# Optimization experiments

Hardware: AMD Instinct MI355X
Metric: run time of the kernel (lower is better)

Reference implementation:

```python
import jax, jax.numpy as jnp
import numpy as np

CHANNEL_DIM = 256
RATE = 4
KSIZE = 2 * RATE - 1  # odd=True


def bilinear_kernel(size, normalize=False):
    factor = (size + 1) // 2
    center = factor - 1 if size % 2 == 1 else factor - 0.5
    og = np.ogrid[:size, :size]
    kern = (1 - abs(og[0] - center) / factor) * (1 - abs(og[1] - center) / factor)
    if normalize:
        kern = kern / kern.sum()
    return kern.astype(np.float32)


def setup_inputs() -> dict:
    key = jax.random.key(0)
    x = jax.random.normal(key, (4, CHANNEL_DIM, 64, 64), dtype=jnp.float32)
    # The torch module builds a [C, C, k, k] weight that is block-diagonal:
    # weight[c, c] = bilinear kernel, all cross-channel blocks are zero.
    # We store only the nonzero diagonal as a depthwise kernel [C, 1, k, k]
    # (OIHW with feature_group_count=C), which computes identical math.
    kern = jnp.asarray(bilinear_kernel(KSIZE, normalize=False))  # [k, k]
    weight = jnp.broadcast_to(kern[None, None], (CHANNEL_DIM, 1, KSIZE, KSIZE))
    return {"x": x, "weight": weight}


def reference(x, weight):
    # F.conv_transpose2d(x, W, stride=r) with no padding/output_padding is
    # equivalent to a cross-correlation of the input dilated by r (lhs_dilation)
    # with the spatially-flipped kernel and padding k-1 on each side.
    # The bilinear kernel is symmetric, so the flip is a no-op.
    k = weight.shape[-1]
    return jax.lax.conv_general_dilated(
        x, weight,
        window_strides=(1, 1),
        padding=((k - 1, k - 1), (k - 1, k - 1)),
        lhs_dilation=(RATE, RATE),
        dimension_numbers=("NCHW", "OIHW", "NCHW"),
        feature_group_count=CHANNEL_DIM,
    )  # -> [N, C, (H-1)*rate + k, (W-1)*rate + k] = [4, 256, 259, 259]
```

## Files before the change

### kernel.cpp

```cpp
#include <hip/hip_runtime.h>


#define IH 64
#define IW 64
#define OH 259
#define OW 259
#define OROW 67081

typedef float float4u __attribute__((ext_vector_type(4), aligned(4)));

__global__ __launch_bounds__(256) void upsample4x_strip(
    const float* __restrict__ x, float* __restrict__ out)
{
    const int lane  = threadIdx.x & 63;
    const int g     = blockIdx.x * 4 + (threadIdx.x >> 6);
    const int strip = g & 7;
    const int nc    = g >> 3;

    const int q0 = strip * 8;
    const int q1 = (strip == 7) ? 65 : q0 + 8;

    const float* __restrict__ xp = x + (size_t)nc * (IH * IW);
    float* __restrict__ ob = out + (size_t)nc * OROW;

    float xl = (q0 == 0) ? 0.0f : xp[(q0 - 1) * IW + lane];
    float xh = xp[q0 * IW + lane];
    float xlm = __shfl_up(xl, 1); if (lane == 0) xlm = 0.0f;
    float xhm = __shfl_up(xh, 1); if (lane == 0) xhm = 0.0f;

    for (int q = q0; q < q1; ++q) {
        const int qn = q + 1;
        float xn = 0.0f;
        if (qn < q1 && qn < IH) xn = xp[qn * IW + lane];

#pragma unroll
        for (int py = 0; py < 4; ++py) {
            const int oy = 4 * q + py;
            if (oy < OH) {
                const float wyl = 0.25f * (float)(3 - py);
                const float wyh = 0.25f * (float)(py + 1);
                float B = wyl * xl  + wyh * xh;
                float A = wyl * xlm + wyh * xhm;

                float e1 = 0.5f * (A + B);
                float e0 = 0.5f * (A + e1);
                float e2 = 0.5f * (e1 + B);

                float* rp = ob + (size_t)oy * OW;
                float4u v = {e0, e1, e2, B};
                ((float4u*)rp)[lane] = v;

                if (lane == 63) {
                    float4u t = {B, 0.75f * B, 0.5f * B, 0.25f * B};
                    *(float4u*)(rp + 255) = t;
                }
            }
        }

        xl = xh; xlm = xhm;
        xh = xn;
        xhm = __shfl_up(xh, 1); if (lane == 0) xhm = 0.0f;
    }
}

extern "C" void kernel_launch(void* const* d_in, const int* in_sizes, int n_in,
                              void* d_out, int out_size, void* d_ws, size_t ws_size,
                              hipStream_t stream)
{
    const float* x = (const float*)d_in[0];
    float* out = (float*)d_out;

    upsample4x_strip<<<2048, 256, 0, stream>>>(x, out);
}
```

Baseline: 301.2 us.

## Distribute row-chunks across waves with grid-stride loop and prefetch

Replaces the per-wave 8-row strip decomposition with a flat work list of (image, input-row) chunks that waves visit in grid-stride order, prefetching the next chunk's two input rows while writing the current four output rows. The aim is to balance work evenly (the old last strip had 9 rows), and to interleave writes across images so more memory channels stay busy. The cost is loading each input row twice (once as lo, once as hi) instead of reusing registers down a strip, plus the division by 65 each iteration.

```diff
diff --git a/kernel.cpp b/kernel.cpp
--- a/kernel.cpp
+++ b/kernel.cpp
@@ -6,60 +6,65 @@
 #define OH 259
 #define OW 259
 #define OROW 67081
+#define NQ 65
+#define NCHUNK (1024 * NQ)
+#define NWAVE 8192
 
 typedef float float4u __attribute__((ext_vector_type(4), aligned(4)));
 
-__global__ __launch_bounds__(256) void upsample4x_strip(
+__global__ __launch_bounds__(256) void upsample4x_chunk(
     const float* __restrict__ x, float* __restrict__ out)
 {
-    const int lane  = threadIdx.x & 63;
-    const int g     = blockIdx.x * 4 + (threadIdx.x >> 6);
-    const int strip = g & 7;
-    const int nc    = g >> 3;
+    const int lane = threadIdx.x & 63;
+    const int w    = blockIdx.x * 4 + (threadIdx.x >> 6);
 
-    const int q0 = strip * 8;
-    const int q1 = (strip == 7) ? 65 : q0 + 8;
+    int c  = w;
+    int nc = c / NQ;
+    int q  = c - nc * NQ;
 
-    const float* __restrict__ xp = x + (size_t)nc * (IH * IW);
-    float* __restrict__ ob = out + (size_t)nc * OROW;
+    float lo = (q > 0)  ? x[(size_t)nc * (IH * IW) + (q - 1) * IW + lane] : 0.0f;
+    float hi = (q < IH) ? x[(size_t)nc * (IH * IW) + q * IW + lane]       : 0.0f;
 
-    float xl = (q0 == 0) ? 0.0f : xp[(q0 - 1) * IW + lane];
-    float xh = xp[q0 * IW + lane];
-    float xlm = __shfl_up(xl, 1); if (lane == 0) xlm = 0.0f;
-    float xhm = __shfl_up(xh, 1); if (lane == 0) xhm = 0.0f;
+    while (true) {
+        const int cn = c + NWAVE;
+        float nlo = 0.0f, nhi = 0.0f;
+        int nnc = 0, nq = 0;
+        if (cn < NCHUNK) {
+            nnc = cn / NQ;
+            nq  = cn - nnc * NQ;
+            const float* xb = x + (size_t)nnc * (IH * IW);
+            if (nq > 0)  nlo = xb[(nq - 1) * IW + lane];
+            if (nq < IH) nhi = xb[nq * IW + lane];
+        }
 
-    for (int q = q0; q < q1; ++q) {
-        const int qn = q + 1;
-        float xn = 0.0f;
-        if (qn < q1 && qn < IH) xn = xp[qn * IW + lane];
+        float lom = __shfl_up(lo, 1); if (lane == 0) lom = 0.0f;
+        float him = __shfl_up(hi, 1); if (lane == 0) him = 0.0f;
 
+        float* rp = out + (size_t)nc * OROW + (size_t)(4 * q) * OW;
 #pragma unroll
         for (int py = 0; py < 4; ++py) {
-            const int oy = 4 * q + py;
-            if (oy < OH) {
+            if (4 * q + py < OH) {
                 const float wyl = 0.25f * (float)(3 - py);
                 const float wyh = 0.25f * (float)(py + 1);
-                float B = wyl * xl  + wyh * xh;
-                float A = wyl * xlm + wyh * xhm;
+                float B = wyl * lo  + wyh * hi;
+                float A = wyl * lom + wyh * him;
 
                 float e1 = 0.5f * (A + B);
                 float e0 = 0.5f * (A + e1);
                 float e2 = 0.5f * (e1 + B);
-
-                float* rp = ob + (size_t)oy * OW;
+                float* rr = rp + (size_t)py * OW;
                 float4u v = {e0, e1, e2, B};
-                ((float4u*)rp)[lane] = v;
+                ((float4u*)rr)[lane] = v;
 
                 if (lane == 63) {
                     float4u t = {B, 0.75f * B, 0.5f * B, 0.25f * B};
-                    *(float4u*)(rp + 255) = t;
+                    *(float4u*)(rr + 255) = t;
                 }
             }
         }
 
-        xl = xh; xlm = xhm;
-        xh = xn;
-        xhm = __shfl_up(xh, 1); if (lane == 0) xhm = 0.0f;
+        if (cn >= NCHUNK) break;
+        c = cn; nc = nnc; q = nq; lo = nlo; hi = nhi;
     }
 }
 
@@ -70,5 +75,5 @@
     const float* x = (const float*)d_in[0];
     float* out = (float*)d_out;
 
-    upsample4x_strip<<<2048, 256, 0, stream>>>(x, out);
+    upsample4x_chunk<<<2048, 256, 0, stream>>>(x, out);
 }
```

New measurement: 299.4 us. No clear change (-0.6%).
